# Kernel optimization log

Measured on AMD Instinct MI355X. Metric: run time of the kernel, lower is better.

Reference implementation:

```python
import jax, jax.numpy as jnp
import numpy as np

NUM_HEADS = 16


def _rotate_half(x):
    x1, x2 = jnp.split(x, 2, axis=-1)
    return jnp.concatenate([-x2, x1], axis=-1)


def _rope_apply(x, sin, cos):
    return x * cos + _rotate_half(x) * sin


def setup_inputs() -> dict:
    key = jax.random.key(0)
    ks = jax.random.split(key, 6)
    B, N, C, HD = 2, 2048, 1024, 64
    x = jax.random.normal(ks[0], (B, N, C), dtype=jnp.float32)
    sin = jax.random.uniform(ks[1], (N - 1, HD), dtype=jnp.float32)
    cos = jax.random.uniform(ks[2], (N - 1, HD), dtype=jnp.float32)
    qkv_w = jax.random.normal(ks[3], (3 * C, C), dtype=jnp.float32) * (C ** -0.5)
    proj_w = jax.random.normal(ks[4], (C, C), dtype=jnp.float32) * (C ** -0.5)
    proj_b = jax.random.normal(ks[5], (C,), dtype=jnp.float32) * 0.02
    return {"x": x, "sin": sin, "cos": cos, "qkv_w": qkv_w,
            "proj_w": proj_w, "proj_b": proj_b}


def reference(x, sin, cos, qkv_w, proj_w, proj_b):
    B, N, C = x.shape
    H = NUM_HEADS
    hd = C // H
    scale = hd ** -0.5

    # QKV projection (no bias): [B,N,3C] -> [B,N,3,H,hd]
    qkv = jnp.einsum('bnc,dc->bnd', x, qkv_w).reshape(B, N, 3, H, hd)
    q = qkv[:, :, 0].transpose(0, 2, 1, 3)  # [B,H,N,hd]
    k = qkv[:, :, 1].transpose(0, 2, 1, 3)
    v = qkv[:, :, 2].transpose(0, 2, 1, 3)

    # RoPE with prefix tokens left unrotated
    prefix = N - sin.shape[0]
    q = jnp.concatenate([q[:, :, :prefix], _rope_apply(q[:, :, prefix:], sin, cos)], axis=2)
    k = jnp.concatenate([k[:, :, :prefix], _rope_apply(k[:, :, prefix:], sin, cos)], axis=2)

    # SDPA (non-causal, no mask)
    scores = jnp.einsum('bhqd,bhkd->bhqk', q, k) * scale
    attn = jax.nn.softmax(scores, axis=-1)
    o = jnp.einsum('bhqk,bhkd->bhqd', attn, v)  # [B,H,N,hd]
    o = o.transpose(0, 2, 1, 3).reshape(B, N, C)

    # Output projection
    return jnp.einsum('bnc,dc->bnd', o, proj_w) + proj_b
```

## Files before the change

kernel.cpp:

```cpp
#include <hip/hip_runtime.h>
#include <hip/hip_bf16.h>
#include <stdint.h>

typedef __hip_bfloat16 bf16;
typedef __attribute__((ext_vector_type(8))) short short8;
typedef __attribute__((ext_vector_type(4))) float floatx4;

#define DEVI static __device__ __forceinline__

typedef __attribute__((address_space(1))) const uint32_t gu32;
typedef __attribute__((address_space(3))) uint32_t lu32;

DEVI void gld_lds16(const void* g, void* l) {
    __builtin_amdgcn_global_load_lds((gu32*)g, (lu32*)l, 16, 0, 0);
}

#define QSCALE 0.18033688011112042f
#define SM_SHIFT 16.0f

__global__ void cvt3_bf16_kernel(const float* __restrict__ s0, bf16* __restrict__ d0, int n0,
                                 const float* __restrict__ s1, bf16* __restrict__ d1, int n1,
                                 const float* __restrict__ s2, bf16* __restrict__ d2, int n2) {
    int c = blockIdx.x * 256 + threadIdx.x;
    const float* src; bf16* dst;
    if (c < n0)           { src = s0; dst = d0; }
    else if (c < n0 + n1) { src = s1; dst = d1; c -= n0; }
    else if (c < n0 + n1 + n2) { src = s2; dst = d2; c -= n0 + n1; }
    else return;
    const int i = c * 4;
    float4 v = *(const float4*)(src + i);
    union { bf16 h[4]; uint2 u; } o;
    o.h[0] = __float2bfloat16(v.x);
    o.h[1] = __float2bfloat16(v.y);
    o.h[2] = __float2bfloat16(v.z);
    o.h[3] = __float2bfloat16(v.w);
    *(uint2*)(dst + i) = o.u;
}

template<int BM, int OUT_BF16, int ADD_BIAS, int SCALE_Q, int ROPE>
__global__ __launch_bounds__(256, 2) void gemm_bt_kernel(
    const bf16* __restrict__ A, const bf16* __restrict__ Bt,
    const float* __restrict__ bias, const float* __restrict__ sinp,
    const float* __restrict__ cosp, void* __restrict__ Cout,
    int M, int N, int K, int nbn)
{
    constexpr int BK = 64;
    constexpr int MFRAG = BM / 32;
    constexpr int ALOADS = BM / 32;
    __shared__ __align__(16) bf16 As[BM * BK];
    __shared__ __align__(16) bf16 Bs[128 * BK];
    const int sb = (blockIdx.x & 7) * ((int)gridDim.x >> 3) + (blockIdx.x >> 3);
    const int bm = sb / nbn;
    const int bn = sb % nbn;
    const int lane = threadIdx.x & 63;
    const int wave = threadIdx.x >> 6;
    const int wm = (wave >> 1) * (BM / 2);
    const int wn = (wave & 1) << 6;

    const int srow = wave * 8 + (lane >> 3);
    const int skc = (((lane & 7) ^ (lane >> 3)) * 8);
    const bf16* Ap = A + (size_t)(bm * BM + srow) * K + skc;
    const bf16* Bp = Bt + (size_t)(bn * 128 + srow) * K + skc;
    bf16* AsD = &As[wave * 512];
    bf16* BsD = &Bs[wave * 512];

    const int frow = lane & 15;
    const int ks   = lane >> 4;

    floatx4 acc[MFRAG][4] = {};

    for (int kt = 0; kt < K; kt += BK) {
#pragma unroll
        for (int s = 0; s < ALOADS; ++s)
            gld_lds16(Ap + kt + (size_t)(32 * s) * K, AsD + 2048 * s);
#pragma unroll
        for (int s = 0; s < 4; ++s)
            gld_lds16(Bp + kt + (size_t)(32 * s) * K, BsD + 2048 * s);
        __syncthreads();
#pragma unroll
        for (int half = 0; half < 2; ++half) {
            short8 af[MFRAG], bfv[4];
#pragma unroll
            for (int m = 0; m < MFRAG; ++m) {
                const int row = wm + m * 16 + frow;
                af[m] = *(const short8*)&As[row * 64 + (((half * 4 + ks) ^ (row & 7)) * 8)];
            }
#pragma unroll
            for (int n = 0; n < 4; ++n) {
                const int row = wn + n * 16 + frow;
                bfv[n] = *(const short8*)&Bs[row * 64 + (((half * 4 + ks) ^ (row & 7)) * 8)];
            }
#pragma unroll
            for (int m = 0; m < MFRAG; ++m)
#pragma unroll
                for (int n = 0; n < 4; ++n)
                    acc[m][n] = __builtin_amdgcn_mfma_f32_16x16x32_bf16(af[m], bfv[n], acc[m][n], 0, 0, 0);
        }
        __syncthreads();
    }

    const int rbase = bm * BM + wm + (lane >> 4) * 4;
    const int cbase = bn * 128 + wn + frow;
#pragma unroll
    for (int m = 0; m < MFRAG; ++m)
#pragma unroll
        for (int r = 0; r < 4; ++r) {
            const int row = rbase + m * 16 + r;
            if (ROPE) {
                const int ntok = row & 2047;
                const int n1 = ntok - 1;
#pragma unroll
                for (int p = 0; p < 2; ++p) {
                    const int colA = cbase + p * 16;
                    const float qs = (SCALE_Q && colA < 1024) ? QSCALE : 1.0f;
                    float vA = acc[m][p][r] * qs;
                    float vB = acc[m][p + 2][r] * qs;
                    if (colA < 2048 && ntok >= 1) {
                        const int j = colA & 63;
                        const int sc = n1 * 64 + j;
                        const float c1 = cosp[sc],      s1 = sinp[sc];
                        const float c2 = cosp[sc + 32], s2 = sinp[sc + 32];
                        const float oA = vA * c1 - vB * s1;
                        const float oB = vB * c2 + vA * s2;
                        vA = oA; vB = oB;
                    }
                    const size_t ia = (size_t)row * N + colA;
                    ((bf16*)Cout)[ia]      = __float2bfloat16(vA);
                    ((bf16*)Cout)[ia + 32] = __float2bfloat16(vB);
                }
            } else {
#pragma unroll
                for (int n = 0; n < 4; ++n) {
                    const int col = cbase + n * 16;
                    const float bv = ADD_BIAS ? bias[col] : 0.f;
                    const float v = acc[m][n][r] + bv;
                    const size_t idx = (size_t)row * N + col;
                    if (OUT_BF16) ((bf16*)Cout)[idx] = __float2bfloat16(v);
                    else          ((float*)Cout)[idx] = v;
                }
            }
        }
}

__global__ __launch_bounds__(512, 4) void attn_kernel(const bf16* __restrict__ qkv,
                                                      bf16* __restrict__ O) {
    __shared__ __align__(16) bf16 Ks[2][2][64 * 64];
    __shared__ __align__(16) bf16 Vt[2][2][64 * 64];

    const int bid = blockIdx.x;
    const int bh = bid & 31;
    const int qt = bid >> 5;
    const int b = bh >> 4;
    const int h = bh & 15;
    const int lane = threadIdx.x & 63;
    const int wave = threadIdx.x >> 6;
    const int t = threadIdx.x;

    const bf16* qb = qkv + (size_t)b * 2048 * 3072 + h * 64;
    const bf16* kb = qb + 1024;
    const bf16* vb = qb + 2048;

    const int frow = lane & 15;
    const int ks   = lane >> 4;
    const int q0   = qt * 128 + wave * 16;

    const bf16* qr = qb + (size_t)(q0 + frow) * 3072;
    const short8 qf0 = *(const short8*)(qr + ks * 8);
    const short8 qf1 = *(const short8*)(qr + 32 + ks * 8);

    short8 vfo = {};
    if (frow == 0) {
        const short one = (short)0x3F80;
#pragma unroll
        for (int j = 0; j < 8; ++j) vfo[j] = one;
    }

    const bool vrole = (wave < 4);

    const int kidx = (wave & 3) * 64 + lane;
    const int kr0 = kidx >> 3, kr1 = (kidx + 256) >> 3;
    const bf16* Kp0 = kb + (size_t)kr0 * 3072 + (((kidx & 7) ^ (kr0 & 7)) * 8);
    const bf16* Kp1 = kb + (size_t)kr1 * 3072 + (((kidx & 7) ^ (kr1 & 7)) * 8);

    const int vkt = wave & 3;
    const int vg  = (t >> 4) & 3;
    const int cb  = t & 15;
    const bf16* Vp = vb + (size_t)(vkt * 16 + vg * 4) * 3072 + cb * 4;
    const int vc = vg + ((vkt >> 1) << 2);
    const int vr = (vkt & 1) * 4;

    floatx4 acc[4] = {};
    floatx4 acc_s = {};

    union VU { ushort4 v; unsigned short e[4]; };
    VU vv[4];

    auto issueV = [&](int k0) {
#pragma unroll
        for (int i = 0; i < 4; ++i)
            vv[i].v = *(const ushort4*)(Vp + (size_t)(k0 + i) * 3072);
    };
    auto writeV = [&](int buf, int sub) {
#pragma unroll
        for (int j = 0; j < 4; ++j) {
            union { unsigned short u[4]; unsigned long long ll; } pk;
#pragma unroll
            for (int i = 0; i < 4; ++i) pk.u[i] = vv[i].e[j];
            const int d = cb * 4 + j;
            const int s = ((d >> 2) & 7) ^ ((d & 3) << 1);
            *(unsigned long long*)&Vt[buf][sub][d * 64 + (((vc ^ s) << 3) + vr)] = pk.ll;
        }
    };
    auto stageK = [&](int k0, int buf, int sub) {
        gld_lds16(Kp0 + (size_t)k0 * 3072, &Ks[buf][sub][(wave & 3) * 512]);
        gld_lds16(Kp1 + (size_t)k0 * 3072, &Ks[buf][sub][(wave & 3) * 512 + 2048]);
    };

    auto compute_tile = [&](int buf, int sub) {
        short8 kf0[4], kf1[4];
#pragma unroll
        for (int kt = 0; kt < 4; ++kt) {
            const int row = kt * 16 + frow;
            kf0[kt] = *(const short8*)&Ks[buf][sub][row * 64 + ((ks ^ (row & 7)) * 8)];
            kf1[kt] = *(const short8*)&Ks[buf][sub][row * 64 + (((ks + 4) ^ (row & 7)) * 8)];
        }
        short8 vf0[4], vf1[4];
#pragma unroll
        for (int dt = 0; dt < 4; ++dt) {
            const int d = dt * 16 + frow;
            const int s = ((d >> 2) & 7) ^ ((d & 3) << 1);
            vf0[dt] = *(const short8*)&Vt[buf][sub][d * 64 + ((ks ^ s) << 3)];
            vf1[dt] = *(const short8*)&Vt[buf][sub][d * 64 + (((ks + 4) ^ s) << 3)];
        }

        floatx4 sv[4];
        __builtin_amdgcn_s_setprio(1);
#pragma unroll
        for (int kt = 0; kt < 4; ++kt) {
            floatx4 z = {-SM_SHIFT, -SM_SHIFT, -SM_SHIFT, -SM_SHIFT};
            z = __builtin_amdgcn_mfma_f32_16x16x32_bf16(kf0[kt], qf0, z, 0, 0, 0);
            z = __builtin_amdgcn_mfma_f32_16x16x32_bf16(kf1[kt], qf1, z, 0, 0, 0);
            sv[kt] = z;
        }
        __builtin_amdgcn_s_setprio(0);

        union PU { __hip_bfloat162 h2[4]; short8 v; };
        PU p0, p1;
#pragma unroll
        for (int kt = 0; kt < 4; ++kt)
#pragma unroll
            for (int m = 0; m < 2; ++m) {
                const float a = __builtin_amdgcn_exp2f(sv[kt][2 * m]);
                const float c = __builtin_amdgcn_exp2f(sv[kt][2 * m + 1]);
                const __hip_bfloat162 pk = __float22bfloat162_rn(float2{a, c});
                if (kt < 2) p0.h2[kt * 2 + m] = pk;
                else        p1.h2[(kt - 2) * 2 + m] = pk;
            }

        __builtin_amdgcn_s_setprio(1);
#pragma unroll
        for (int dt = 0; dt < 4; ++dt) {
            acc[dt] = __builtin_amdgcn_mfma_f32_16x16x32_bf16(p0.v, vf0[dt], acc[dt], 0, 0, 0);
            acc[dt] = __builtin_amdgcn_mfma_f32_16x16x32_bf16(p1.v, vf1[dt], acc[dt], 0, 0, 0);
        }
        acc_s = __builtin_amdgcn_mfma_f32_16x16x32_bf16(p0.v, vfo, acc_s, 0, 0, 0);
        acc_s = __builtin_amdgcn_mfma_f32_16x16x32_bf16(p1.v, vfo, acc_s, 0, 0, 0);
        __builtin_amdgcn_s_setprio(0);
    };

    if (vrole) {
        issueV(0);  writeV(0, 0);
        issueV(64); writeV(0, 1);
    } else {
        stageK(0, 0, 0);
        stageK(64, 0, 1);
    }
    __syncthreads();

    for (int tt = 0; tt < 16; ++tt) {
        const int cur = tt & 1, nxt = cur ^ 1;
        const int k0 = tt * 128;
        const bool pf = tt < 15;
        if (pf) {
            if (vrole) issueV(k0 + 128);
            else { stageK(k0 + 128, nxt, 0); stageK(k0 + 192, nxt, 1); }
        }
        compute_tile(cur, 0);
        if (pf && vrole) { writeV(nxt, 0); issueV(k0 + 192); }
        compute_tile(cur, 1);
        if (pf && vrole) writeV(nxt, 1);
        __syncthreads();
    }

    floatx4 li;
#pragma unroll
    for (int i = 0; i < 4; ++i) li[i] = 1.0f / __shfl(acc_s[i], lane & 48);
    const int nrow = q0 + (lane >> 4) * 4;
#pragma unroll
    for (int i = 0; i < 4; ++i) {
        const size_t base = ((size_t)b * 2048 + nrow + i) * 1024 + h * 64 + frow;
#pragma unroll
        for (int dt = 0; dt < 4; ++dt)
            O[base + dt * 16] = __float2bfloat16(acc[dt][i] * li[i]);
    }
}

extern "C" void kernel_launch(void* const* d_in, const int* in_sizes, int n_in,
                              void* d_out, int out_size, void* d_ws, size_t ws_size,
                              hipStream_t stream) {
    const float* x      = (const float*)d_in[0];
    const float* sinp   = (const float*)d_in[1];
    const float* cosp   = (const float*)d_in[2];
    const float* qkv_w  = (const float*)d_in[3];
    const float* proj_w = (const float*)d_in[4];
    const float* proj_b = (const float*)d_in[5];
    float* out = (float*)d_out;

    char* ws = (char*)d_ws;
    bf16* xb    = (bf16*)(ws);
    bf16* wqkv  = (bf16*)(ws + 8388608);
    bf16* wproj = (bf16*)(ws + 8388608 + 6291456);
    bf16* qkvb  = (bf16*)(ws + 16777216);
    bf16* attno = (bf16*)(ws + 16777216 + 25165824);

    cvt3_bf16_kernel<<<(1048576 + 786432 + 262144) / 256, 256, 0, stream>>>(
        x, xb, 1048576, qkv_w, wqkv, 786432, proj_w, wproj, 262144);

    gemm_bt_kernel<128, 1, 0, 1, 1><<<32 * 24, 256, 0, stream>>>(
        xb, wqkv, nullptr, sinp, cosp, qkvb, 4096, 3072, 1024, 24);
    attn_kernel<<<512, 512, 0, stream>>>(qkvb, attno);
    gemm_bt_kernel<64, 0, 1, 0, 0><<<64 * 8, 256, 0, stream>>>(
        attno, wproj, proj_b, nullptr, nullptr, out, 4096, 1024, 1024, 8);
}
```

Measured before the change: 122.3 us.

## Spread K and V staging across all waves instead of role-split waves

In the attention kernel, all 8 waves now share the K async-to-LDS loads and the V transpose loads, where before waves 0-3 did V and waves 4-7 did K. Each wave issues one K load per sub-tile and one V sub-tile per iteration, with a sched_barrier placed before the V global loads. The aim is to balance load work across waves so no wave group stalls the block barrier. The trade-off is that every wave now carries V register traffic and LDS writes, which may interfere with its compute.

Result: faster. 111.6 us (-8.8%).

```diff
diff --git a/kernel.cpp b/kernel.cpp
--- a/kernel.cpp
+++ b/kernel.cpp
@@ -154,7 +154,6 @@
     const int h = bh & 15;
     const int lane = threadIdx.x & 63;
     const int wave = threadIdx.x >> 6;
-    const int t = threadIdx.x;
 
     const bf16* qb = qkv + (size_t)b * 2048 * 3072 + h * 64;
     const bf16* kb = qb + 1024;
@@ -175,17 +174,15 @@
         for (int j = 0; j < 8; ++j) vfo[j] = one;
     }
 
-    const bool vrole = (wave < 4);
-
-    const int kidx = (wave & 3) * 64 + lane;
-    const int kr0 = kidx >> 3, kr1 = (kidx + 256) >> 3;
-    const bf16* Kp0 = kb + (size_t)kr0 * 3072 + (((kidx & 7) ^ (kr0 & 7)) * 8);
-    const bf16* Kp1 = kb + (size_t)kr1 * 3072 + (((kidx & 7) ^ (kr1 & 7)) * 8);
-
-    const int vkt = wave & 3;
-    const int vg  = (t >> 4) & 3;
-    const int cb  = t & 15;
-    const bf16* Vp = vb + (size_t)(vkt * 16 + vg * 4) * 3072 + cb * 4;
+    const int kidx = wave * 64 + lane;
+    const int krow = kidx >> 3;
+    const bf16* Kp = kb + (size_t)krow * 3072 + (((kidx & 7) ^ (krow & 7)) * 8);
+
+    const int vsub = wave >> 2;
+    const int vkt  = wave & 3;
+    const int vg   = (lane >> 4) & 3;
+    const int cb   = lane & 15;
+    const bf16* Vp = vb + (size_t)(vsub * 64 + vkt * 16 + vg * 4) * 3072 + cb * 4;
     const int vc = vg + ((vkt >> 1) << 2);
     const int vr = (vkt & 1) * 4;
 
@@ -195,12 +192,15 @@
     union VU { ushort4 v; unsigned short e[4]; };
     VU vv[4];
 
+    auto stageK = [&](int k0, int buf, int sub) {
+        gld_lds16(Kp + (size_t)k0 * 3072, &Ks[buf][sub][wave * 512]);
+    };
     auto issueV = [&](int k0) {
 #pragma unroll
         for (int i = 0; i < 4; ++i)
             vv[i].v = *(const ushort4*)(Vp + (size_t)(k0 + i) * 3072);
     };
-    auto writeV = [&](int buf, int sub) {
+    auto writeV = [&](int buf) {
 #pragma unroll
         for (int j = 0; j < 4; ++j) {
             union { unsigned short u[4]; unsigned long long ll; } pk;
@@ -208,12 +208,8 @@
             for (int i = 0; i < 4; ++i) pk.u[i] = vv[i].e[j];
             const int d = cb * 4 + j;
             const int s = ((d >> 2) & 7) ^ ((d & 3) << 1);
-            *(unsigned long long*)&Vt[buf][sub][d * 64 + (((vc ^ s) << 3) + vr)] = pk.ll;
-        }
-    };
-    auto stageK = [&](int k0, int buf, int sub) {
-        gld_lds16(Kp0 + (size_t)k0 * 3072, &Ks[buf][sub][(wave & 3) * 512]);
-        gld_lds16(Kp1 + (size_t)k0 * 3072, &Ks[buf][sub][(wave & 3) * 512 + 2048]);
+            *(unsigned long long*)&Vt[buf][vsub][d * 64 + (((vc ^ s) << 3) + vr)] = pk.ll;
+        }
     };
 
     auto compute_tile = [&](int buf, int sub) {
@@ -268,27 +264,25 @@
         __builtin_amdgcn_s_setprio(0);
     };
 
-    if (vrole) {
-        issueV(0);  writeV(0, 0);
-        issueV(64); writeV(0, 1);
-    } else {
-        stageK(0, 0, 0);
-        stageK(64, 0, 1);
-    }
+    stageK(0, 0, 0);
+    stageK(64, 0, 1);
+    issueV(0);
+    writeV(0);
     __syncthreads();
 
     for (int tt = 0; tt < 16; ++tt) {
         const int cur = tt & 1, nxt = cur ^ 1;
-        const int k0 = tt * 128;
+        const int knext = (tt + 1) * 128;
         const bool pf = tt < 15;
         if (pf) {
-            if (vrole) issueV(k0 + 128);
-            else { stageK(k0 + 128, nxt, 0); stageK(k0 + 192, nxt, 1); }
+            stageK(knext, nxt, 0);
+            stageK(knext + 64, nxt, 1);
         }
         compute_tile(cur, 0);
-        if (pf && vrole) { writeV(nxt, 0); issueV(k0 + 192); }
+        __builtin_amdgcn_sched_barrier(0);
+        if (pf) issueV(knext);
         compute_tile(cur, 1);
-        if (pf && vrole) writeV(nxt, 1);
+        if (pf) writeV(nxt);
         __syncthreads();
     }
 
```
